# Kernel tuning notes

Measured on AMD Instinct MI355X. Metric: run time of the kernel, lower is better.

Reference implementation:

```python
import jax, jax.numpy as jnp
import numpy as np

D_MODEL = 4096
N_HEADS = 32
KV_HEADS = 8
HEAD_DIM = D_MODEL // N_HEADS  # 128
GROUPS = N_HEADS // KV_HEADS   # 4
ROPE_THETA = 500000.0
CLIP_QKV = 8.0
SEQLENS = [512, 768, 384, 384]
T = sum(SEQLENS)  # 2048 total ragged tokens


def setup_inputs() -> dict:
    key = jax.random.key(0)
    k1, k2, k3 = jax.random.split(key, 3)
    hidden_states = jax.random.normal(k1, (T, D_MODEL), dtype=jnp.float32)
    # fused Wqkv: rows = d_model (Q) + 2 * kv_heads * head_dim (K,V)
    w_qkv = jax.random.normal(k2, (D_MODEL + 2 * KV_HEADS * HEAD_DIM, D_MODEL), dtype=jnp.float32) * 0.02
    w_o = jax.random.normal(k3, (D_MODEL, D_MODEL), dtype=jnp.float32) * 0.02
    # ragged-batch metadata: cumulative sequence lengths, per-token positions
    cu = np.concatenate([[0], np.cumsum(SEQLENS)]).astype(np.int32)
    pos = np.concatenate([np.arange(l) for l in SEQLENS]).astype(np.float32)
    inv_freq = 1.0 / (ROPE_THETA ** (np.arange(0, HEAD_DIM, 2, dtype=np.float32) / HEAD_DIM))  # [64]
    freqs = pos[:, None] * inv_freq[None, :]  # [T, 64]
    return {
        "hidden_states": hidden_states,
        "w_qkv": w_qkv,
        "w_o": w_o,
        "cos": jnp.asarray(np.cos(freqs), dtype=jnp.float32),
        "sin": jnp.asarray(np.sin(freqs), dtype=jnp.float32),
        "cu_seqlens": jnp.asarray(cu),
    }


def _rope(x, cos, sin):
    # rotate-half (NeoX-style) RoPE, as in TGI PositionRotaryEmbedding
    h = HEAD_DIM // 2
    x1, x2 = x[..., :h], x[..., h:]
    c = cos[:, None, :]  # [T,1,h] broadcast over heads
    s = sin[:, None, :]
    return jnp.concatenate([x1 * c - x2 * s, x2 * c + x1 * s], axis=-1)


def reference(hidden_states, w_qkv, w_o, cos, sin, cu_seqlens):
    # fused QKV projection + clip_qkv clamp
    qkv = jnp.clip(hidden_states @ w_qkv.T, -CLIP_QKV, CLIP_QKV)  # [T, 6144]
    q_sz = N_HEADS * HEAD_DIM
    kv_sz = KV_HEADS * HEAD_DIM
    q = qkv[:, :q_sz].reshape(T, N_HEADS, HEAD_DIM)
    k = qkv[:, q_sz:q_sz + kv_sz].reshape(T, KV_HEADS, HEAD_DIM)
    v = qkv[:, q_sz + kv_sz:].reshape(T, KV_HEADS, HEAD_DIM)
    q = _rope(q, cos, sin)
    k = _rope(k, cos, sin)
    # GQA: expand kv heads to query heads (kv_head_mapping = repeat_interleave)
    kr = jnp.repeat(k, GROUPS, axis=1)  # [T, H, D]
    vr = jnp.repeat(v, GROUPS, axis=1)
    # varlen causal mask: same segment AND key index <= query index
    idx = jnp.arange(T)
    seg = jnp.searchsorted(cu_seqlens, idx, side="right") - 1  # [T]
    mask = (seg[:, None] == seg[None, :]) & (idx[:, None] >= idx[None, :])  # [T,T]
    scale = HEAD_DIM ** -0.5
    scores = jnp.einsum("qhd,khd->hqk", q, kr) * scale  # [H,T,T]
    scores = jnp.where(mask[None, :, :], scores, jnp.finfo(scores.dtype).min)
    attn = jax.nn.softmax(scores, axis=-1)
    out = jnp.einsum("hqk,khd->qhd", attn, vr).reshape(T, N_HEADS * HEAD_DIM)
    return out @ w_o.T
```

## Files before the change

### kernel.cpp

```cpp
#include <hip/hip_runtime.h>

#define T_TOK 2048
#define DM    4096
#define NH    32
#define KVH   8
#define HD    128
#define QKV_N 6144
#define KOFF  4096
#define VOFF  5120
#define SCALE 0.08838834764831845f

typedef __attribute__((ext_vector_type(8))) short  short8;
typedef __attribute__((ext_vector_type(4))) float  floatx4;

__device__ __forceinline__ ushort f2bf(float f) {
  union { float f; unsigned u; } x; x.f = f;
  unsigned u = x.u;
  return (ushort)((u + 0x7fffu + ((u >> 16) & 1u)) >> 16);
}
__device__ __forceinline__ float bf2f(ushort h) {
  union { unsigned u; float f; } x; x.u = ((unsigned)h) << 16;
  return x.f;
}

__global__ void __launch_bounds__(256) cast_bf16_kernel(const float* __restrict__ x,
                                                        ushort* __restrict__ y, int n4) {
  int i = blockIdx.x * 256 + threadIdx.x;
  if (i >= n4) return;
  float4 v = ((const float4*)x)[i];
  ushort4 o;
  o.x = f2bf(v.x); o.y = f2bf(v.y); o.z = f2bf(v.z); o.w = f2bf(v.w);
  ((ushort4*)y)[i] = o;
}

__device__ __forceinline__ void gld_lds16(const ushort* g, ushort* l) {
  __builtin_amdgcn_global_load_lds((const __attribute__((address_space(1))) unsigned int*)g,
                                   (__attribute__((address_space(3))) unsigned int*)l,
                                   16, 0, 0);
}

__global__ void __launch_bounds__(256) gemm_bt(const ushort* __restrict__ A,
                                               const ushort* __restrict__ B,
                                               ushort* __restrict__ Cb,
                                               float* __restrict__ Cf,
                                               int N, int K, int mode) {
  __shared__ ushort As[128 * 32];
  __shared__ ushort Bs[128 * 32];
  const int tid = threadIdx.x, wave = tid >> 6, lane = tid & 63;
  const int bm = blockIdx.y * 128, bn = blockIdx.x * 128;
  const int wr = (wave >> 1) * 64, wc = (wave & 1) * 64;
  const int r = lane & 15, g = lane >> 4;

  floatx4 zero = {0.f, 0.f, 0.f, 0.f};
  floatx4 acc[4][4];
#pragma unroll
  for (int mi = 0; mi < 4; mi++)
#pragma unroll
    for (int ni = 0; ni < 4; ni++) acc[mi][ni] = zero;

  const ushort* Ag = A + (size_t)(bm + wave * 32 + (lane >> 2)) * K + (lane & 3) * 8;
  const ushort* Bg = B + (size_t)(bn + wave * 32 + (lane >> 2)) * K + (lane & 3) * 8;
  ushort* Al = &As[(wave * 32) * 32];
  ushort* Bl = &Bs[(wave * 32) * 32];

  for (int k0 = 0; k0 < K; k0 += 32) {
    gld_lds16(Ag,          Al);
    gld_lds16(Ag + 16 * K, Al + 16 * 32);
    gld_lds16(Bg,          Bl);
    gld_lds16(Bg + 16 * K, Bl + 16 * 32);
    Ag += 32; Bg += 32;
    __syncthreads();

    short8 af[4], bfr[4];
#pragma unroll
    for (int i = 0; i < 4; i++) af[i]  = *(const short8*)&As[(wr + i * 16 + r) * 32 + g * 8];
#pragma unroll
    for (int i = 0; i < 4; i++) bfr[i] = *(const short8*)&Bs[(wc + i * 16 + r) * 32 + g * 8];
#pragma unroll
    for (int mi = 0; mi < 4; mi++)
#pragma unroll
      for (int ni = 0; ni < 4; ni++)
        acc[mi][ni] = __builtin_amdgcn_mfma_f32_16x16x32_bf16(af[mi], bfr[ni], acc[mi][ni], 0, 0, 0);
    __syncthreads();
  }

#pragma unroll
  for (int mi = 0; mi < 4; mi++)
#pragma unroll
    for (int v = 0; v < 4; v++) {
      int row = bm + wr + mi * 16 + g * 4 + v;
#pragma unroll
      for (int ni = 0; ni < 4; ni++) {
        int col = bn + wc + ni * 16 + r;
        float x = acc[mi][ni][v];
        if (mode == 0) {
          x = fminf(8.0f, fmaxf(-8.0f, x));
          Cb[(size_t)row * N + col] = f2bf(x);
        } else {
          Cf[(size_t)row * N + col] = x;
        }
      }
    }
}

__global__ void __launch_bounds__(256) rope_kernel(ushort* __restrict__ qkv,
                                                   const float* __restrict__ cosb,
                                                   const float* __restrict__ sinb) {
  int t = blockIdx.y;
  int h = blockIdx.x * 4 + (threadIdx.x >> 6);
  int d = threadIdx.x & 63;
  size_t base = (size_t)t * QKV_N + (h < NH ? h * HD : KOFF + (h - NH) * HD);
  float x1 = bf2f(qkv[base + d]);
  float x2 = bf2f(qkv[base + 64 + d]);
  float c = cosb[t * 64 + d], s = sinb[t * 64 + d];
  float y1 = x1 * c - x2 * s;
  float y2 = x2 * c + x1 * s;
  if (h < NH) { y1 *= SCALE; y2 *= SCALE; }
  qkv[base + d]      = f2bf(y1);
  qkv[base + 64 + d] = f2bf(y2);
}

__global__ void __launch_bounds__(256) vtrans_kernel(const ushort* __restrict__ qkv,
                                                     ushort* __restrict__ vt) {
  int idx = blockIdx.x * 256 + threadIdx.x;
  int t  = idx & (T_TOK - 1);
  int d  = (idx >> 11) & (HD - 1);
  int kv = idx >> 18;
  vt[idx] = qkv[(size_t)t * QKV_N + VOFF + kv * HD + d];
}

__global__ void __launch_bounds__(256) attn_kernel(const ushort* __restrict__ qkv,
                                                   const ushort* __restrict__ vt,
                                                   ushort* __restrict__ o) {
  __shared__ ushort Ks[64][136];
  __shared__ ushort Vts[128][72];
  __shared__ ushort Ps[4][16][72];

  const int tid = threadIdx.x, wave = tid >> 6, lane = tid & 63;
  const int r = lane & 15, g = lane >> 4;
  const int qtile = blockIdx.x, head = blockIdx.y, kvh = head >> 2;
  const int q0 = qtile * 64;
  int s0;
  if (q0 < 512) s0 = 0; else if (q0 < 1280) s0 = 512;
  else if (q0 < 1664) s0 = 1280; else s0 = 1664;

  short8 qf[4];
  const int qrow = q0 + wave * 16 + r;
#pragma unroll
  for (int ks = 0; ks < 4; ks++)
    qf[ks] = *(const short8*)&qkv[(size_t)qrow * QKV_N + head * HD + ks * 32 + g * 8];

  floatx4 zero = {0.f, 0.f, 0.f, 0.f};
  floatx4 oacc[8];
#pragma unroll
  for (int b = 0; b < 8; b++) oacc[b] = zero;
  float mrun[4] = {-1e30f, -1e30f, -1e30f, -1e30f};
  float lrun[4] = {0.f, 0.f, 0.f, 0.f};

  const size_t kcol  = (size_t)KOFF + kvh * HD;
  const size_t vbase = (size_t)kvh * HD * T_TOK;

  for (int k0 = s0; k0 < q0 + 64; k0 += 64) {
    short8 kreg[4], vreg[4];
#pragma unroll
    for (int p = 0; p < 4; p++) {
      int krow = p * 16 + (tid >> 4), kc = (tid & 15) * 8;
      kreg[p] = *(const short8*)&qkv[(size_t)(k0 + krow) * QKV_N + kcol + kc];
      int vd = p * 32 + (tid >> 3), vc = (tid & 7) * 8;
      vreg[p] = *(const short8*)&vt[vbase + (size_t)vd * T_TOK + k0 + vc];
    }
    __syncthreads();
#pragma unroll
    for (int p = 0; p < 4; p++) {
      int krow = p * 16 + (tid >> 4), kc = (tid & 15) * 8;
      *(short8*)&Ks[krow][kc] = kreg[p];
      int vd = p * 32 + (tid >> 3), vc = (tid & 7) * 8;
      *(short8*)&Vts[vd][vc] = vreg[p];
    }
    __syncthreads();

    floatx4 sacc[4];
#pragma unroll
    for (int s = 0; s < 4; s++) sacc[s] = zero;
#pragma unroll
    for (int s = 0; s < 4; s++)
#pragma unroll
      for (int ks = 0; ks < 4; ks++) {
        short8 kf = *(const short8*)&Ks[s * 16 + r][ks * 32 + g * 8];
        sacc[s] = __builtin_amdgcn_mfma_f32_16x16x32_bf16(qf[ks], kf, sacc[s], 0, 0, 0);
      }

    const bool diag = (k0 == q0);
    float sv[4][4];
#pragma unroll
    for (int s = 0; s < 4; s++)
#pragma unroll
      for (int v = 0; v < 4; v++) {
        float x = sacc[s][v];
        if (diag) {
          int ka = k0 + s * 16 + r;
          int qa = q0 + wave * 16 + g * 4 + v;
          if (ka > qa) x = -1e30f;
        }
        sv[s][v] = x;
      }

    float rmax[4];
#pragma unroll
    for (int v = 0; v < 4; v++)
      rmax[v] = fmaxf(fmaxf(sv[0][v], sv[1][v]), fmaxf(sv[2][v], sv[3][v]));
#pragma unroll
    for (int off = 1; off < 16; off <<= 1)
#pragma unroll
      for (int v = 0; v < 4; v++)
        rmax[v] = fmaxf(rmax[v], __shfl_xor(rmax[v], off, 64));

    float newm[4], alpha[4];
#pragma unroll
    for (int v = 0; v < 4; v++) {
      newm[v]  = fmaxf(mrun[v], rmax[v]);
      alpha[v] = __expf(mrun[v] - newm[v]);
      mrun[v]  = newm[v];
    }

    float pv[4][4];
    float rsum[4] = {0.f, 0.f, 0.f, 0.f};
#pragma unroll
    for (int s = 0; s < 4; s++)
#pragma unroll
      for (int v = 0; v < 4; v++) {
        float p = __expf(sv[s][v] - newm[v]);
        pv[s][v] = p;
        rsum[v] += p;
      }
#pragma unroll
    for (int off = 1; off < 16; off <<= 1)
#pragma unroll
      for (int v = 0; v < 4; v++)
        rsum[v] += __shfl_xor(rsum[v], off, 64);
#pragma unroll
    for (int v = 0; v < 4; v++) lrun[v] = lrun[v] * alpha[v] + rsum[v];
#pragma unroll
    for (int b = 0; b < 8; b++)
#pragma unroll
      for (int v = 0; v < 4; v++) oacc[b][v] *= alpha[v];

#pragma unroll
    for (int s = 0; s < 4; s++)
#pragma unroll
      for (int v = 0; v < 4; v++)
        Ps[wave][g * 4 + v][s * 16 + r] = f2bf(pv[s][v]);
    __syncthreads();

    short8 pf0 = *(const short8*)&Ps[wave][r][g * 8];
    short8 pf1 = *(const short8*)&Ps[wave][r][32 + g * 8];

#pragma unroll
    for (int b = 0; b < 8; b++) {
      short8 v0 = *(const short8*)&Vts[b * 16 + r][g * 8];
      short8 v1 = *(const short8*)&Vts[b * 16 + r][32 + g * 8];
      oacc[b] = __builtin_amdgcn_mfma_f32_16x16x32_bf16(pf0, v0, oacc[b], 0, 0, 0);
      oacc[b] = __builtin_amdgcn_mfma_f32_16x16x32_bf16(pf1, v1, oacc[b], 0, 0, 0);
    }
  }

  float rinv[4];
#pragma unroll
  for (int v = 0; v < 4; v++) rinv[v] = 1.0f / lrun[v];
#pragma unroll
  for (int b = 0; b < 8; b++)
#pragma unroll
    for (int v = 0; v < 4; v++) {
      int qa = q0 + wave * 16 + g * 4 + v;
      o[(size_t)qa * DM + head * HD + b * 16 + r] = f2bf(oacc[b][v] * rinv[v]);
    }
}

extern "C" void kernel_launch(void* const* d_in, const int* in_sizes, int n_in,
                              void* d_out, int out_size, void* d_ws, size_t ws_size,
                              hipStream_t stream) {
  const float* hs   = (const float*)d_in[0];
  const float* wqkv = (const float*)d_in[1];
  const float* wo   = (const float*)d_in[2];
  const float* cosb = (const float*)d_in[3];
  const float* sinb = (const float*)d_in[4];
  float* out = (float*)d_out;

  char* w = (char*)d_ws;
  ushort* h_bf   = (ushort*)(w);
  ushort* wq_bf  = (ushort*)(w + 16777216);
  ushort* wo_bf  = (ushort*)(w + 67108864);
  ushort* qkv_bf = (ushort*)(w + 100663296);
  ushort* vt     = (ushort*)(w + 125829120);
  ushort* ao_bf  = (ushort*)(w + 130023424);

  cast_bf16_kernel<<<8192,  256, 0, stream>>>(hs,   h_bf,  2097152);
  cast_bf16_kernel<<<24576, 256, 0, stream>>>(wqkv, wq_bf, 6291456);
  cast_bf16_kernel<<<16384, 256, 0, stream>>>(wo,   wo_bf, 4194304);

  gemm_bt<<<dim3(48, 16), 256, 0, stream>>>(h_bf, wq_bf, qkv_bf, nullptr, QKV_N, DM, 0);
  rope_kernel<<<dim3(10, T_TOK), 256, 0, stream>>>(qkv_bf, cosb, sinb);
  vtrans_kernel<<<8192, 256, 0, stream>>>(qkv_bf, vt);
  attn_kernel<<<dim3(32, 32), 256, 0, stream>>>(qkv_bf, vt, ao_bf);
  gemm_bt<<<dim3(32, 16), 256, 0, stream>>>(ao_bf, wo_bf, nullptr, out, DM, DM, 1);
}
```

Before: 562.2 us.

## Replace GEMM with 256x256-tile double-buffered swizzled-LDS pipelined kernel

Replaces the 128x128, single-buffered GEMM with a 256x256 tile kernel using 8 waves, K-step 64 and double-buffered LDS. Global-to-LDS loads for future tiles are issued between quarter-blocks of MFMAs. LDS columns are XOR-swizzled to avoid bank conflicts, wave priority is raised around the MFMA bursts, and workgroup IDs are remapped across XCDs. The aim is to hide memory latency and raise tensor-core utilisation on both projections. The cost is heavier register and LDS use and fewer workgroups (192 and 128), which can leave CUs idle.

```diff
diff --git a/kernel.cpp b/kernel.cpp
--- a/kernel.cpp
+++ b/kernel.cpp
@@ -39,59 +39,139 @@
                                    16, 0, 0);
 }
 
-__global__ void __launch_bounds__(256) gemm_bt(const ushort* __restrict__ A,
-                                               const ushort* __restrict__ B,
-                                               ushort* __restrict__ Cb,
-                                               float* __restrict__ Cf,
-                                               int N, int K, int mode) {
-  __shared__ ushort As[128 * 32];
-  __shared__ ushort Bs[128 * 32];
-  const int tid = threadIdx.x, wave = tid >> 6, lane = tid & 63;
-  const int bm = blockIdx.y * 128, bn = blockIdx.x * 128;
-  const int wr = (wave >> 1) * 64, wc = (wave & 1) * 64;
+__device__ __forceinline__ void bar() {
+  asm volatile("" ::: "memory");
+  __builtin_amdgcn_s_barrier();
+  asm volatile("" ::: "memory");
+}
+
+template <int MLO, int NLO>
+__device__ __forceinline__ void mfma_quad(floatx4 (&acc)[8][4],
+                                          const short8 (&afr)[4][2],
+                                          const short8 (&bfr)[4][2]) {
+  __builtin_amdgcn_s_setprio(1);
+#pragma unroll
+  for (int ks = 0; ks < 2; ++ks)
+#pragma unroll
+    for (int mi = 0; mi < 4; ++mi)
+#pragma unroll
+      for (int ni = 0; ni < 2; ++ni)
+        acc[MLO + mi][NLO + ni] = __builtin_amdgcn_mfma_f32_16x16x32_bf16(
+            afr[mi][ks], bfr[NLO + ni][ks], acc[MLO + mi][NLO + ni], 0, 0, 0);
+  __builtin_amdgcn_s_setprio(0);
+}
+
+__device__ __forceinline__ void stage_half(const ushort* __restrict__ G, size_t row0,
+                                           int K, int k0, ushort* lbase, int tid) {
+#pragma unroll
+  for (int j = 0; j < 2; ++j) {
+    int row   = j * 64 + (tid >> 3);
+    int chunk = (tid & 7) ^ (row & 7);
+    gld_lds16(G + (row0 + (size_t)row) * K + k0 + chunk * 8,
+              lbase + (size_t)(j * 512 + tid) * 8);
+  }
+}
+
+__global__ void __launch_bounds__(512, 2)
+gemm256(const ushort* __restrict__ A, const ushort* __restrict__ B,
+        ushort* __restrict__ Cb, float* __restrict__ Cf, int N, int K, int mode) {
+  __shared__ __align__(16) ushort As[2][2][128][64];
+  __shared__ __align__(16) ushort Bs[2][2][128][64];
+
+  const int tid = threadIdx.x;
+  const int lane = tid & 63, wv = tid >> 6;
   const int r = lane & 15, g = lane >> 4;
-
-  floatx4 zero = {0.f, 0.f, 0.f, 0.f};
-  floatx4 acc[4][4];
-#pragma unroll
-  for (int mi = 0; mi < 4; mi++)
-#pragma unroll
-    for (int ni = 0; ni < 4; ni++) acc[mi][ni] = zero;
-
-  const ushort* Ag = A + (size_t)(bm + wave * 32 + (lane >> 2)) * K + (lane & 3) * 8;
-  const ushort* Bg = B + (size_t)(bn + wave * 32 + (lane >> 2)) * K + (lane & 3) * 8;
-  ushort* Al = &As[(wave * 32) * 32];
-  ushort* Bl = &Bs[(wave * 32) * 32];
-
-  for (int k0 = 0; k0 < K; k0 += 32) {
-    gld_lds16(Ag,          Al);
-    gld_lds16(Ag + 16 * K, Al + 16 * 32);
-    gld_lds16(Bg,          Bl);
-    gld_lds16(Bg + 16 * K, Bl + 16 * 32);
-    Ag += 32; Bg += 32;
-    __syncthreads();
-
-    short8 af[4], bfr[4];
-#pragma unroll
-    for (int i = 0; i < 4; i++) af[i]  = *(const short8*)&As[(wr + i * 16 + r) * 32 + g * 8];
-#pragma unroll
-    for (int i = 0; i < 4; i++) bfr[i] = *(const short8*)&Bs[(wc + i * 16 + r) * 32 + g * 8];
-#pragma unroll
-    for (int mi = 0; mi < 4; mi++)
-#pragma unroll
-      for (int ni = 0; ni < 4; ni++)
-        acc[mi][ni] = __builtin_amdgcn_mfma_f32_16x16x32_bf16(af[mi], bfr[ni], acc[mi][ni], 0, 0, 0);
-    __syncthreads();
+  const int wm = wv >> 2, wn = wv & 3;
+
+  const int nwg = (int)gridDim.x;
+  const int wg  = (int)blockIdx.x;
+  const int wgs = (wg & 7) * (nwg >> 3) + (wg >> 3);
+  const int nbx = N >> 8;
+  const int bx = wgs % nbx, by = wgs / nbx;
+  const int bm = by * 256, bn = bx * 256;
+
+  const int NT = K >> 6;
+
+  floatx4 acc[8][4];
+#pragma unroll
+  for (int mi = 0; mi < 8; ++mi)
+#pragma unroll
+    for (int ni = 0; ni < 4; ++ni) acc[mi][ni] = (floatx4){0.f, 0.f, 0.f, 0.f};
+
+  stage_half(B, bn,       K, 0, &Bs[0][0][0][0], tid);
+  stage_half(B, bn + 128, K, 0, &Bs[0][1][0][0], tid);
+  stage_half(A, bm,       K, 0, &As[0][0][0][0], tid);
+  stage_half(A, bm + 128, K, 0, &As[0][1][0][0], tid);
+  if (NT > 1) {
+    stage_half(B, bn,       K, 64, &Bs[1][0][0][0], tid);
+    stage_half(B, bn + 128, K, 64, &Bs[1][1][0][0], tid);
+    stage_half(A, bm,       K, 64, &As[1][0][0][0], tid);
+    asm volatile("s_waitcnt vmcnt(6)" ::: "memory");
+  } else {
+    asm volatile("s_waitcnt vmcnt(0)" ::: "memory");
   }
-
-#pragma unroll
-  for (int mi = 0; mi < 4; mi++)
-#pragma unroll
-    for (int v = 0; v < 4; v++) {
-      int row = bm + wr + mi * 16 + g * 4 + v;
-#pragma unroll
-      for (int ni = 0; ni < 4; ni++) {
-        int col = bn + wc + ni * 16 + r;
+  bar();
+
+  short8 afr[4][2], bfr[4][2];
+  const int cswz = (r & 7) << 3;
+
+  for (int t = 0; t < NT; ++t) {
+    const int buf = t & 1;
+    const ushort* Ab = &As[buf][wm][0][0];
+    const ushort* Bb = &Bs[buf][wn >> 1][0][0];
+    const int brow = (wn & 1) * 64;
+
+#pragma unroll
+    for (int ni = 0; ni < 4; ++ni)
+#pragma unroll
+      for (int ks = 0; ks < 2; ++ks)
+        bfr[ni][ks] = *(const short8*)&Bb[(brow + ni * 16 + r) * 64 +
+                                          ((ks * 32 + g * 8) ^ cswz)];
+#pragma unroll
+    for (int m = 0; m < 4; ++m)
+#pragma unroll
+      for (int ks = 0; ks < 2; ++ks)
+        afr[m][ks] = *(const short8*)&Ab[(m * 16 + r) * 64 +
+                                         ((ks * 32 + g * 8) ^ cswz)];
+    if (t + 1 < NT) stage_half(A, bm + 128, K, (t + 1) * 64, &As[(t + 1) & 1][1][0][0], tid);
+    asm volatile("s_waitcnt lgkmcnt(0)" ::: "memory");
+    bar();
+    mfma_quad<0, 0>(acc, afr, bfr);
+    bar();
+
+    if (t + 2 < NT) stage_half(B, bn, K, (t + 2) * 64, &Bs[buf][0][0][0], tid);
+    bar();
+    mfma_quad<0, 2>(acc, afr, bfr);
+    bar();
+
+#pragma unroll
+    for (int m = 0; m < 4; ++m)
+#pragma unroll
+      for (int ks = 0; ks < 2; ++ks)
+        afr[m][ks] = *(const short8*)&Ab[((64 + m * 16) + r) * 64 +
+                                         ((ks * 32 + g * 8) ^ cswz)];
+    if (t + 2 < NT) stage_half(B, bn + 128, K, (t + 2) * 64, &Bs[buf][1][0][0], tid);
+    asm volatile("s_waitcnt lgkmcnt(0)" ::: "memory");
+    bar();
+    mfma_quad<4, 2>(acc, afr, bfr);
+    bar();
+
+    if (t + 2 < NT) stage_half(A, bm, K, (t + 2) * 64, &As[buf][0][0][0], tid);
+    if (t < NT - 2) asm volatile("s_waitcnt vmcnt(6)" ::: "memory");
+    else            asm volatile("s_waitcnt vmcnt(0)" ::: "memory");
+    bar();
+    mfma_quad<4, 0>(acc, afr, bfr);
+    bar();
+  }
+
+#pragma unroll
+  for (int mi = 0; mi < 8; ++mi)
+#pragma unroll
+    for (int v = 0; v < 4; ++v) {
+      int row = bm + wm * 128 + mi * 16 + g * 4 + v;
+#pragma unroll
+      for (int ni = 0; ni < 4; ++ni) {
+        int col = bn + wn * 64 + ni * 16 + r;
         float x = acc[mi][ni][v];
         if (mode == 0) {
           x = fminf(8.0f, fmaxf(-8.0f, x));
@@ -298,9 +378,9 @@
   cast_bf16_kernel<<<24576, 256, 0, stream>>>(wqkv, wq_bf, 6291456);
   cast_bf16_kernel<<<16384, 256, 0, stream>>>(wo,   wo_bf, 4194304);
 
-  gemm_bt<<<dim3(48, 16), 256, 0, stream>>>(h_bf, wq_bf, qkv_bf, nullptr, QKV_N, DM, 0);
+  gemm256<<<dim3(192), 512, 0, stream>>>(h_bf, wq_bf, qkv_bf, nullptr, QKV_N, DM, 0);
   rope_kernel<<<dim3(10, T_TOK), 256, 0, stream>>>(qkv_bf, cosb, sinb);
   vtrans_kernel<<<8192, 256, 0, stream>>>(qkv_bf, vt);
   attn_kernel<<<dim3(32, 32), 256, 0, stream>>>(qkv_bf, vt, ao_bf);
-  gemm_bt<<<dim3(32, 16), 256, 0, stream>>>(ao_bf, wo_bf, nullptr, out, DM, DM, 1);
-}
+  gemm256<<<dim3(128), 512, 0, stream>>>(ao_bf, wo_bf, nullptr, out, DM, DM, 1);
+}
```

Result: slower. 576.1 us (+2.5%).
